# Kernel optimization log

Measured on AMD Instinct MI355X. Metric: run time of the kernel, lower is better.

Reference implementation:

```python
import jax, jax.numpy as jnp
import numpy as np

DIM = 768
HEADS = 12
DIM_HEAD = 64
INNER = HEADS * DIM_HEAD  # 768
B, N = 8, 1024


def layernorm(x, gamma, beta, eps=1e-5):
    mu = jnp.mean(x, axis=-1, keepdims=True)
    var = jnp.var(x, axis=-1, keepdims=True)
    return (x - mu) * jax.lax.rsqrt(var + eps) * gamma + beta


def setup_inputs() -> dict:
    key = jax.random.key(0)
    ks = jax.random.split(key, 12)
    s = lambda fan_in: 1.0 / np.sqrt(fan_in)
    return {
        "x": jax.random.normal(ks[0], (B, N, DIM), dtype=jnp.float32),
        "ln1_g": jnp.ones((DIM,), jnp.float32),
        "ln1_b": jnp.zeros((DIM,), jnp.float32),
        "ln2_g": jnp.ones((DIM,), jnp.float32),
        "ln2_b": jnp.zeros((DIM,), jnp.float32),
        "w_qkv": jax.random.uniform(ks[1], (DIM, 3 * INNER), jnp.float32, -s(DIM), s(DIM)),
        "w_out": jax.random.uniform(ks[2], (INNER, DIM), jnp.float32, -s(INNER), s(INNER)),
        "b_out": jax.random.uniform(ks[3], (DIM,), jnp.float32, -s(INNER), s(INNER)),
        "w_ff1": jax.random.uniform(ks[4], (DIM, 4 * DIM), jnp.float32, -s(DIM), s(DIM)),
        "b_ff1": jax.random.uniform(ks[5], (4 * DIM,), jnp.float32, -s(DIM), s(DIM)),
        "w_ff2": jax.random.uniform(ks[6], (4 * DIM, DIM), jnp.float32, -s(4 * DIM), s(4 * DIM)),
        "b_ff2": jax.random.uniform(ks[7], (DIM,), jnp.float32, -s(4 * DIM), s(4 * DIM)),
    }


def reference(x, ln1_g, ln1_b, ln2_g, ln2_b, w_qkv, w_out, b_out, w_ff1, b_ff1, w_ff2, b_ff2):
    # --- attention sub-block (dropout = identity, eval mode) ---
    residual = x
    h = layernorm(x, ln1_g, ln1_b)
    qkv = h @ w_qkv  # [B, N, 3*INNER]
    q, k, v = jnp.split(qkv, 3, axis=-1)
    # b n (h d) -> b h n d
    reshape = lambda t: t.reshape(B, N, HEADS, DIM_HEAD).transpose(0, 2, 1, 3)
    q, k, v = reshape(q), reshape(k), reshape(v)
    scale = DIM_HEAD ** -0.5
    attn = jnp.einsum('bhnd,bhmd->bhnm', q, k) * scale
    attn = jax.nn.softmax(attn, axis=-1)
    out = jnp.einsum('bhnm,bhmd->bhnd', attn, v)
    out = out.transpose(0, 2, 1, 3).reshape(B, N, INNER)  # b h n d -> b n (h d)
    out = out @ w_out + b_out
    x = residual + out
    # --- FFN sub-block ---
    h2 = layernorm(x, ln2_g, ln2_b)
    ff = jax.nn.gelu(h2 @ w_ff1 + b_ff1, approximate=False) @ w_ff2 + b_ff2
    return x + ff
```

## Files before the change

kernel.cpp:

```cpp
#include <hip/hip_runtime.h>
#include <hip/hip_bf16.h>
#include <math.h>
#include <stdint.h>

#define BATCH 8
#define SEQ   1024
#define DIM   768
#define HEADS 12
#define DHEAD 64
#define TOK   (BATCH*SEQ)
#define INNER 768
#define FFDIM 3072
#define QKVN  2304
#define QKLD  1536

typedef float floatx4 __attribute__((ext_vector_type(4)));
typedef __bf16 bf16x8 __attribute__((ext_vector_type(8)));

__device__ __forceinline__ float b2f(uint16_t u) {
    return __uint_as_float(((uint32_t)u) << 16);
}
__device__ __forceinline__ uint16_t f2b(float f) {
    uint32_t x = __float_as_uint(f);
    x += 0x7fffu + ((x >> 16) & 1u);
    return (uint16_t)(x >> 16);
}
__device__ __forceinline__ uint32_t cvt_pk_bf16(float lo, float hi) {
    uint32_t r;
    asm("v_cvt_pk_bf16_f32 %0, %1, %2" : "=v"(r) : "v"(lo), "v"(hi));
    return r;
}

__device__ __forceinline__ void gload_lds16(const uint16_t* g, uint16_t* l) {
    __builtin_amdgcn_global_load_lds(
        (const __attribute__((address_space(1))) uint32_t*)g,
        (__attribute__((address_space(3))) uint32_t*)l, 16, 0, 0);
}

__global__ __launch_bounds__(256) void transpose_convert(
    const float* __restrict__ in, uint16_t* __restrict__ outT, int R, int C)
{
    __shared__ float tile[32][33];
    int c0 = blockIdx.x * 32, r0 = blockIdx.y * 32;
    int x = threadIdx.x;
    int y = threadIdx.y;
    #pragma unroll
    for (int i = y; i < 32; i += 8)
        tile[i][x] = in[(size_t)(r0 + i) * C + c0 + x];
    __syncthreads();
    #pragma unroll
    for (int i = y; i < 32; i += 8)
        outT[(size_t)(c0 + i) * R + r0 + x] = f2b(tile[x][i]);
}

__global__ __launch_bounds__(64) void ln_naive(
    const float* __restrict__ x, const float* __restrict__ g,
    const float* __restrict__ be, uint16_t* __restrict__ y)
{
    const int lane = threadIdx.x;
    const size_t row = blockIdx.x;
    float v[12];
    float s = 0.f, ss = 0.f;
    #pragma unroll
    for (int j = 0; j < 12; j++) {
        int idx = lane + j * 64;
        float f = x[row * DIM + idx];
        v[j] = f; s += f; ss += f * f;
    }
    #pragma unroll
    for (int off = 32; off > 0; off >>= 1) {
        s  += __shfl_xor(s, off);
        ss += __shfl_xor(ss, off);
    }
    const float mu = s * (1.f / DIM);
    const float var = ss * (1.f / DIM) - mu * mu;
    const float rstd = rsqrtf(var + 1e-5f);
    #pragma unroll
    for (int j = 0; j < 12; j++) {
        int idx = lane + j * 64;
        y[row * DIM + idx] = f2b((v[j] - mu) * rstd * g[idx] + be[idx]);
    }
}

#define GEMM_STAGE(buf, kk) do {                                                            \
    _Pragma("unroll")                                                                       \
    for (int i = 0; i < 2; i++) {                                                           \
        int row = i * 64 + srow;                                                            \
        gload_lds16(A  + (size_t)(tileM + row) * lda  + (kk) + scol, &a_tile[buf][row * 32 + scol]); \
        gload_lds16(Bt + (size_t)(tileN + row) * ldbt + (kk) + scol, &b_tile[buf][row * 32 + scol]); \
    } } while (0)

template<bool BIAS, bool GELU, bool RES, bool OUTF, bool VSPLIT>
__global__ __launch_bounds__(256) void gemm_bt(
    const uint16_t* __restrict__ A, const uint16_t* __restrict__ Bt,
    void* C, const float* __restrict__ bias, int bias_off,
    const float* res, int N, int K, int lda, int ldbt, int ldc,
    uint16_t* __restrict__ vt)
{
    __shared__ __align__(16) uint16_t a_tile[2][128 * 32];
    __shared__ __align__(16) uint16_t b_tile[2][128 * 32];
    const int tid = threadIdx.x;
    const int wave = tid >> 6, lane = tid & 63;
    const int wr = wave >> 1, wc = wave & 1;

    const int nwg = gridDim.x * gridDim.y;
    int bid = blockIdx.y * gridDim.x + blockIdx.x;
    if ((nwg & 7) == 0)
        bid = (bid & 7) * (nwg >> 3) + (bid >> 3);
    const int tileM = (bid / gridDim.x) * 128;
    const int tileN = (bid % gridDim.x) * 128;

    floatx4 acc[4][4] = {};

    const int scol = (tid & 3) * 8;
    const int srow = tid >> 2;
    const int lm = lane & 15;
    const int lq = lane >> 4;
    const int kq = lq * 8;

    GEMM_STAGE(0, 0);
    asm volatile("s_waitcnt vmcnt(0)" ::: "memory");
    __syncthreads();

    int cur = 0;
    for (int k0 = 0; k0 < K; k0 += 32) {
        if (k0 + 32 < K) GEMM_STAGE(cur ^ 1, k0 + 32);

        bf16x8 af[4], bfr[4];
        #pragma unroll
        for (int rt = 0; rt < 4; rt++) {
            int r = wr * 64 + rt * 16 + lm;
            af[rt] = *(const bf16x8*)&a_tile[cur][r * 32 + kq];
        }
        #pragma unroll
        for (int nt = 0; nt < 4; nt++) {
            int n = wc * 64 + nt * 16 + lm;
            bfr[nt] = *(const bf16x8*)&b_tile[cur][n * 32 + kq];
        }
        #pragma unroll
        for (int rt = 0; rt < 4; rt++)
            #pragma unroll
            for (int nt = 0; nt < 4; nt++)
                acc[rt][nt] = __builtin_amdgcn_mfma_f32_16x16x32_bf16(
                    af[rt], bfr[nt], acc[rt][nt], 0, 0, 0);

        __syncthreads();
        cur ^= 1;
    }

    const bool vpath = VSPLIT && (tileN >= 1536);
    #pragma unroll
    for (int rt = 0; rt < 4; rt++) {
        int r0 = tileM + wr * 64 + rt * 16 + lq * 4;
        #pragma unroll
        for (int nt = 0; nt < 4; nt++) {
            int cg = tileN + wc * 64 + nt * 16 + lm;
            if (vpath) {
                int d = cg - 1536;
                int bb = r0 >> 10, s0 = r0 & 1023;
                uint32_t p0 = (uint32_t)f2b(acc[rt][nt][0]) | ((uint32_t)f2b(acc[rt][nt][1]) << 16);
                uint32_t p1 = (uint32_t)f2b(acc[rt][nt][2]) | ((uint32_t)f2b(acc[rt][nt][3]) << 16);
                uint2 pk; pk.x = p0; pk.y = p1;
                *(uint2*)&vt[((size_t)bb * 768 + d) * 1024 + s0] = pk;
            } else {
                float bvv = BIAS ? bias[bias_off + cg] : 0.f;
                #pragma unroll
                for (int r = 0; r < 4; r++) {
                    float v = acc[rt][nt][r] + bvv;
                    if (GELU) v = 0.5f * v * (1.f + erff(v * 0.70710678118f));
                    size_t ci = (size_t)(r0 + r) * ldc + cg;
                    if (RES) v += res[ci];
                    if (OUTF) ((float*)C)[ci] = v;
                    else      ((uint16_t*)C)[ci] = f2b(v);
                }
            }
        }
    }
}

#define KSWZ(row, cb) ((cb) ^ (((row) & 7) << 4))
#define NKT (SEQ / 64)

__global__ __launch_bounds__(256) void flash_mfma(
    uint16_t* qk, const uint16_t* __restrict__ vt)
{
    __shared__ __align__(16) uint16_t k_s[64 * 64];
    __shared__ __align__(16) uint16_t v_s[64 * 64];
    __shared__ __align__(16) uint16_t p_s[64 * 64];
    char* k_c = (char*)k_s;
    char* v_c = (char*)v_s;
    char* p_c = (char*)p_s;

    const int t = threadIdx.x;
    const int wq = t >> 6;
    const int lane = t & 63;
    const int lm = lane & 15;
    const int lq = lane >> 4;

    const int qb = blockIdx.x, h = blockIdx.y, b = blockIdx.z;
    const size_t rowbase = (size_t)b * SEQ;
    const int hcol = h * DHEAD;

    bf16x8 qf[2];
    {
        const uint16_t* qp = qk + (rowbase + qb*64 + wq*16 + lm) * QKLD + hcol + lq*8;
        qf[0] = *(const bf16x8*)qp;
        qf[1] = *(const bf16x8*)(qp + 32);
    }

    floatx4 O[4] = {};
    float m_q = -1e30f, l_q = 0.f;

    const int s_row = t >> 2;
    const int s_cb  = (t & 3) * 32;
    const size_t kgbase = (rowbase + s_row) * QKLD + INNER + hcol;
    const size_t vgbase = ((size_t)b * 768 + hcol + s_row) * 1024;

    uint4 kr0, kr1, vr0, vr1;
    {
        const char* kp = (const char*)(qk + kgbase);
        kr0 = *(const uint4*)(kp + s_cb);
        kr1 = *(const uint4*)(kp + s_cb + 16);
        const char* vp = (const char*)(vt + vgbase);
        vr0 = *(const uint4*)(vp + s_cb);
        vr1 = *(const uint4*)(vp + s_cb + 16);
    }

    for (int kt = 0; kt < NKT; ++kt) {
        *(uint4*)&k_c[s_row*128 + KSWZ(s_row, s_cb)]      = kr0;
        *(uint4*)&k_c[s_row*128 + KSWZ(s_row, s_cb + 16)] = kr1;
        *(uint4*)&v_c[s_row*128 + KSWZ(s_row, s_cb)]      = vr0;
        *(uint4*)&v_c[s_row*128 + KSWZ(s_row, s_cb + 16)] = vr1;
        __syncthreads();

        if (kt + 1 < NKT) {
            const char* kp = (const char*)(qk + kgbase + (size_t)(kt + 1) * 64 * QKLD);
            kr0 = *(const uint4*)(kp + s_cb);
            kr1 = *(const uint4*)(kp + s_cb + 16);
            const char* vp = (const char*)(vt + vgbase + (size_t)(kt + 1) * 64);
            vr0 = *(const uint4*)(vp + s_cb);
            vr1 = *(const uint4*)(vp + s_cb + 16);
        }

        floatx4 S[4];
        #pragma unroll
        for (int nt = 0; nt < 4; nt++) {
            const int row = nt*16 + lm;
            bf16x8 ak0 = *(const bf16x8*)&k_c[row*128 + KSWZ(row, lq*16)];
            bf16x8 ak1 = *(const bf16x8*)&k_c[row*128 + KSWZ(row, 64 + lq*16)];
            floatx4 a = {};
            a = __builtin_amdgcn_mfma_f32_16x16x32_bf16(ak0, qf[0], a, 0, 0, 0);
            a = __builtin_amdgcn_mfma_f32_16x16x32_bf16(ak1, qf[1], a, 0, 0, 0);
            S[nt] = a;
        }

        float m0 = fmaxf(fmaxf(S[0][0], S[0][1]), fmaxf(S[0][2], S[0][3]));
        float m1 = fmaxf(fmaxf(S[1][0], S[1][1]), fmaxf(S[1][2], S[1][3]));
        float m2 = fmaxf(fmaxf(S[2][0], S[2][1]), fmaxf(S[2][2], S[2][3]));
        float m3 = fmaxf(fmaxf(S[3][0], S[3][1]), fmaxf(S[3][2], S[3][3]));
        float mx = fmaxf(fmaxf(m0, m1), fmaxf(m2, m3)) * 0.125f;
        mx = fmaxf(mx, __shfl_xor(mx, 16));
        mx = fmaxf(mx, __shfl_xor(mx, 32));
        const float mn = fmaxf(m_q, mx);
        const float alpha = __expf(m_q - mn);
        m_q = mn;

        float p[4][4];
        float sum = 0.f;
        #pragma unroll
        for (int nt = 0; nt < 4; nt++) {
            float p0 = __expf(S[nt][0] * 0.125f - mn);
            float p1 = __expf(S[nt][1] * 0.125f - mn);
            float p2 = __expf(S[nt][2] * 0.125f - mn);
            float p3 = __expf(S[nt][3] * 0.125f - mn);
            p[nt][0] = p0; p[nt][1] = p1; p[nt][2] = p2; p[nt][3] = p3;
            sum += (p0 + p1) + (p2 + p3);
        }
        sum += __shfl_xor(sum, 16);
        sum += __shfl_xor(sum, 32);
        l_q = l_q * alpha + sum;

        const int prow = wq*16 + lm;
        #pragma unroll
        for (int nt = 0; nt < 4; nt++) {
            uint2 w;
            w.x = cvt_pk_bf16(p[nt][0], p[nt][1]);
            w.y = cvt_pk_bf16(p[nt][2], p[nt][3]);
            *(uint2*)&p_c[prow*128 + KSWZ(prow, nt*32 + lq*8)] = w;
        }

        #pragma unroll
        for (int nt = 0; nt < 4; nt++) {
            O[nt][0] *= alpha; O[nt][1] *= alpha;
            O[nt][2] *= alpha; O[nt][3] *= alpha;
        }

        #pragma unroll
        for (int ks = 0; ks < 2; ks++) {
            bf16x8 bp = *(const bf16x8*)&p_c[prow*128 + KSWZ(prow, ks*64 + lq*16)];
            #pragma unroll
            for (int nt = 0; nt < 4; nt++) {
                const int vrow = nt*16 + lm;
                bf16x8 av = *(const bf16x8*)&v_c[vrow*128 + KSWZ(vrow, ks*64 + lq*16)];
                O[nt] = __builtin_amdgcn_mfma_f32_16x16x32_bf16(av, bp, O[nt], 0, 0, 0);
            }
        }
        __syncthreads();
    }

    const float linv = 1.f / l_q;
    uint16_t* dst = qk + (rowbase + qb*64 + wq*16 + lm) * QKLD + hcol;
    #pragma unroll
    for (int nt = 0; nt < 4; nt++) {
        uint2 w;
        w.x = cvt_pk_bf16(O[nt][0] * linv, O[nt][1] * linv);
        w.y = cvt_pk_bf16(O[nt][2] * linv, O[nt][3] * linv);
        *(uint2*)&dst[nt*16 + lq*4] = w;
    }
}

extern "C" void kernel_launch(void* const* d_in, const int* in_sizes, int n_in,
                              void* d_out, int out_size, void* d_ws, size_t ws_size,
                              hipStream_t stream) {
    const float* x      = (const float*)d_in[0];
    const float* ln1_g  = (const float*)d_in[1];
    const float* ln1_b  = (const float*)d_in[2];
    const float* ln2_g  = (const float*)d_in[3];
    const float* ln2_b  = (const float*)d_in[4];
    const float* w_qkv  = (const float*)d_in[5];
    const float* w_out  = (const float*)d_in[6];
    const float* b_out  = (const float*)d_in[7];
    const float* w_ff1  = (const float*)d_in[8];
    const float* b_ff1  = (const float*)d_in[9];
    const float* w_ff2  = (const float*)d_in[10];
    const float* b_ff2  = (const float*)d_in[11];
    float* out = (float*)d_out;

    uint16_t* ws  = (uint16_t*)d_ws;
    uint16_t* qk  = ws;
    uint16_t* ffc = ws;
    uint16_t* vT  = ws + (size_t)12582912;
    uint16_t* h   = ws + (size_t)18874368;
    uint16_t* WqT = ws + (size_t)25165824;
    uint16_t* WoT = ws + (size_t)26935296;
    uint16_t* W1T = ws + (size_t)27525120;
    uint16_t* W2T = ws + (size_t)29884416;

    dim3 tb(32, 8);
    hipLaunchKernelGGL(transpose_convert, dim3(QKVN/32, DIM/32), tb, 0, stream, w_qkv, WqT, DIM, QKVN);
    hipLaunchKernelGGL(transpose_convert, dim3(DIM/32,  DIM/32), tb, 0, stream, w_out, WoT, DIM, DIM);
    hipLaunchKernelGGL(transpose_convert, dim3(FFDIM/32, DIM/32), tb, 0, stream, w_ff1, W1T, DIM, FFDIM);
    hipLaunchKernelGGL(transpose_convert, dim3(DIM/32, FFDIM/32), tb, 0, stream, w_ff2, W2T, FFDIM, DIM);

    hipLaunchKernelGGL(ln_naive, dim3(TOK), dim3(64), 0, stream, x, ln1_g, ln1_b, h);
    hipLaunchKernelGGL((gemm_bt<false, false, false, false, true>), dim3(QKVN/128, TOK/128), dim3(256), 0, stream,
                       h, WqT, qk, nullptr, 0, nullptr, QKVN, DIM, DIM, DIM, QKLD, vT);
    hipLaunchKernelGGL(flash_mfma, dim3(SEQ/64, HEADS, BATCH), dim3(256), 0, stream, qk, vT);
    hipLaunchKernelGGL((gemm_bt<true, false, true, true, false>), dim3(DIM/128, TOK/128), dim3(256), 0, stream,
                       qk, WoT, out, b_out, 0, x, DIM, INNER, QKLD, DIM, DIM, nullptr);
    hipLaunchKernelGGL(ln_naive, dim3(TOK), dim3(64), 0, stream, out, ln2_g, ln2_b, h);
    for (int c = 0; c < 2; c++) {
        hipLaunchKernelGGL((gemm_bt<true, true, false, false, false>), dim3(1536/128, TOK/128), dim3(256), 0, stream,
                           h, W1T + (size_t)c*1536*DIM, ffc, b_ff1, c*1536, nullptr,
                           1536, DIM, DIM, DIM, 1536, nullptr);
        if (c == 0) {
            hipLaunchKernelGGL((gemm_bt<true, false, true, true, false>), dim3(DIM/128, TOK/128), dim3(256), 0, stream,
                               ffc, W2T + (size_t)c*1536, out, b_ff2, 0, out,
                               DIM, 1536, 1536, FFDIM, DIM, nullptr);
        } else {
            hipLaunchKernelGGL((gemm_bt<false, false, true, true, false>), dim3(DIM/128, TOK/128), dim3(256), 0, stream,
                               ffc, W2T + (size_t)c*1536, out, nullptr, 0, out,
                               DIM, 1536, 1536, FFDIM, DIM, nullptr);
        }
    }
}
```

Before: 443.9 us.

## Double-buffer flash attention LDS, lazy softmax rescale, exp2 math, cheaper GELU erf

The flash attention kernel now double-buffers its K/V shared-memory tiles, so each key tile needs one barrier instead of two. Softmax moves to base-2 with the scale folded into one FMA, uses raw v_exp/v_rcp, and skips the output rescale unless the running max grows past a threshold. Blocks are remapped so neighbouring work is spread across XCDs, for better L2 locality. The FFN GELU swaps erff for an Abramowitz-Stegun polynomial using fast exp and reciprocal, which cuts transcendental cost at a small accuracy cost.

```diff
diff --git a/kernel.cpp b/kernel.cpp
--- a/kernel.cpp
+++ b/kernel.cpp
@@ -29,6 +29,23 @@
     uint32_t r;
     asm("v_cvt_pk_bf16_f32 %0, %1, %2" : "=v"(r) : "v"(lo), "v"(hi));
     return r;
+}
+__device__ __forceinline__ float exp2_fast(float x) {
+    float r; asm("v_exp_f32 %0, %1" : "=v"(r) : "v"(x)); return r;
+}
+__device__ __forceinline__ float rcp_fast(float x) {
+    float r; asm("v_rcp_f32 %0, %1" : "=v"(r) : "v"(x)); return r;
+}
+
+__device__ __forceinline__ float gelu_exact(float v) {
+    float x  = v * 0.70710678f;
+    float ax = fabsf(x);
+    float t  = rcp_fast(fmaf(0.3275911f, ax, 1.0f));
+    float poly = t * fmaf(t, fmaf(t, fmaf(t, fmaf(t, 1.061405429f, -1.453152027f),
+                          1.421413741f), -0.284496736f), 0.254829592f);
+    float e = 1.0f - poly * exp2_fast(x * x * -1.44269504f);
+    float erfv = copysignf(e, x);
+    return 0.5f * v * (1.0f + erfv);
 }
 
 __device__ __forceinline__ void gload_lds16(const uint16_t* g, uint16_t* l) {
@@ -167,7 +184,7 @@
                 #pragma unroll
                 for (int r = 0; r < 4; r++) {
                     float v = acc[rt][nt][r] + bvv;
-                    if (GELU) v = 0.5f * v * (1.f + erff(v * 0.70710678118f));
+                    if (GELU) v = gelu_exact(v);
                     size_t ci = (size_t)(r0 + r) * ldc + cg;
                     if (RES) v += res[ci];
                     if (OUTF) ((float*)C)[ci] = v;
@@ -180,16 +197,18 @@
 
 #define KSWZ(row, cb) ((cb) ^ (((row) & 7) << 4))
 #define NKT (SEQ / 64)
+#define SM_C   0.18033688f
+#define SM_THR 11.5416f
 
 __global__ __launch_bounds__(256) void flash_mfma(
     uint16_t* qk, const uint16_t* __restrict__ vt)
 {
-    __shared__ __align__(16) uint16_t k_s[64 * 64];
-    __shared__ __align__(16) uint16_t v_s[64 * 64];
+    __shared__ __align__(16) uint16_t k_s[2][64 * 64];
+    __shared__ __align__(16) uint16_t v_s[2][64 * 64];
     __shared__ __align__(16) uint16_t p_s[64 * 64];
-    char* k_c = (char*)k_s;
-    char* v_c = (char*)v_s;
-    char* p_c = (char*)p_s;
+    char* k_base = (char*)k_s;
+    char* v_base = (char*)v_s;
+    char* p_c    = (char*)p_s;
 
     const int t = threadIdx.x;
     const int wq = t >> 6;
@@ -197,7 +216,13 @@
     const int lm = lane & 15;
     const int lq = lane >> 4;
 
-    const int qb = blockIdx.x, h = blockIdx.y, b = blockIdx.z;
+    int flat = blockIdx.x + 16 * (blockIdx.y + 12 * blockIdx.z);
+    int nw = (flat & 7) * 192 + (flat >> 3);
+    const int b  = nw / 192;
+    const int rem = nw - b * 192;
+    const int h  = rem >> 4;
+    const int qb = rem & 15;
+
     const size_t rowbase = (size_t)b * SEQ;
     const int hcol = h * DHEAD;
 
@@ -224,13 +249,14 @@
         const char* vp = (const char*)(vt + vgbase);
         vr0 = *(const uint4*)(vp + s_cb);
         vr1 = *(const uint4*)(vp + s_cb + 16);
-    }
-
+        *(uint4*)&k_base[s_row*128 + KSWZ(s_row, s_cb)]      = kr0;
+        *(uint4*)&k_base[s_row*128 + KSWZ(s_row, s_cb + 16)] = kr1;
+        *(uint4*)&v_base[s_row*128 + KSWZ(s_row, s_cb)]      = vr0;
+        *(uint4*)&v_base[s_row*128 + KSWZ(s_row, s_cb + 16)] = vr1;
+    }
+
+    int cur = 0;
     for (int kt = 0; kt < NKT; ++kt) {
-        *(uint4*)&k_c[s_row*128 + KSWZ(s_row, s_cb)]      = kr0;
-        *(uint4*)&k_c[s_row*128 + KSWZ(s_row, s_cb + 16)] = kr1;
-        *(uint4*)&v_c[s_row*128 + KSWZ(s_row, s_cb)]      = vr0;
-        *(uint4*)&v_c[s_row*128 + KSWZ(s_row, s_cb + 16)] = vr1;
         __syncthreads();
 
         if (kt + 1 < NKT) {
@@ -241,6 +267,9 @@
             vr0 = *(const uint4*)(vp + s_cb);
             vr1 = *(const uint4*)(vp + s_cb + 16);
         }
+
+        const char* k_c = k_base + cur * 8192;
+        const char* v_c = v_base + cur * 8192;
 
         floatx4 S[4];
         #pragma unroll
@@ -258,27 +287,37 @@
         float m1 = fmaxf(fmaxf(S[1][0], S[1][1]), fmaxf(S[1][2], S[1][3]));
         float m2 = fmaxf(fmaxf(S[2][0], S[2][1]), fmaxf(S[2][2], S[2][3]));
         float m3 = fmaxf(fmaxf(S[3][0], S[3][1]), fmaxf(S[3][2], S[3][3]));
-        float mx = fmaxf(fmaxf(m0, m1), fmaxf(m2, m3)) * 0.125f;
+        float mx = fmaxf(fmaxf(m0, m1), fmaxf(m2, m3)) * SM_C;
         mx = fmaxf(mx, __shfl_xor(mx, 16));
         mx = fmaxf(mx, __shfl_xor(mx, 32));
-        const float mn = fmaxf(m_q, mx);
-        const float alpha = __expf(m_q - mn);
-        m_q = mn;
+
+        float mn = m_q;
+        if (!__all(mx <= m_q + SM_THR)) {
+            mn = fmaxf(m_q, mx);
+            float alpha = exp2_fast(m_q - mn);
+            m_q = mn;
+            l_q *= alpha;
+            #pragma unroll
+            for (int nt = 0; nt < 4; nt++) {
+                O[nt][0] *= alpha; O[nt][1] *= alpha;
+                O[nt][2] *= alpha; O[nt][3] *= alpha;
+            }
+        }
 
         float p[4][4];
         float sum = 0.f;
         #pragma unroll
         for (int nt = 0; nt < 4; nt++) {
-            float p0 = __expf(S[nt][0] * 0.125f - mn);
-            float p1 = __expf(S[nt][1] * 0.125f - mn);
-            float p2 = __expf(S[nt][2] * 0.125f - mn);
-            float p3 = __expf(S[nt][3] * 0.125f - mn);
+            float p0 = exp2_fast(fmaf(S[nt][0], SM_C, -mn));
+            float p1 = exp2_fast(fmaf(S[nt][1], SM_C, -mn));
+            float p2 = exp2_fast(fmaf(S[nt][2], SM_C, -mn));
+            float p3 = exp2_fast(fmaf(S[nt][3], SM_C, -mn));
             p[nt][0] = p0; p[nt][1] = p1; p[nt][2] = p2; p[nt][3] = p3;
             sum += (p0 + p1) + (p2 + p3);
         }
         sum += __shfl_xor(sum, 16);
         sum += __shfl_xor(sum, 32);
-        l_q = l_q * alpha + sum;
+        l_q += sum;
 
         const int prow = wq*16 + lm;
         #pragma unroll
@@ -287,12 +326,6 @@
             w.x = cvt_pk_bf16(p[nt][0], p[nt][1]);
             w.y = cvt_pk_bf16(p[nt][2], p[nt][3]);
             *(uint2*)&p_c[prow*128 + KSWZ(prow, nt*32 + lq*8)] = w;
-        }
-
-        #pragma unroll
-        for (int nt = 0; nt < 4; nt++) {
-            O[nt][0] *= alpha; O[nt][1] *= alpha;
-            O[nt][2] *= alpha; O[nt][3] *= alpha;
         }
 
         #pragma unroll
@@ -305,10 +338,19 @@
                 O[nt] = __builtin_amdgcn_mfma_f32_16x16x32_bf16(av, bp, O[nt], 0, 0, 0);
             }
         }
-        __syncthreads();
-    }
-
-    const float linv = 1.f / l_q;
+
+        if (kt + 1 < NKT) {
+            char* kn = k_base + (cur ^ 1) * 8192;
+            char* vn = v_base + (cur ^ 1) * 8192;
+            *(uint4*)&kn[s_row*128 + KSWZ(s_row, s_cb)]      = kr0;
+            *(uint4*)&kn[s_row*128 + KSWZ(s_row, s_cb + 16)] = kr1;
+            *(uint4*)&vn[s_row*128 + KSWZ(s_row, s_cb)]      = vr0;
+            *(uint4*)&vn[s_row*128 + KSWZ(s_row, s_cb + 16)] = vr1;
+        }
+        cur ^= 1;
+    }
+
+    const float linv = rcp_fast(l_q);
     uint16_t* dst = qk + (rowbase + qb*64 + wq*16 + lm) * QKLD + hcol;
     #pragma unroll
     for (int nt = 0; nt < 4; nt++) {
```

After: 432.3 us. -2.6%, faster.
